# Kernel tuning notes

Hardware: AMD Instinct MI355X
Metric: run time of the kernel (lower is better)

The kernel has to match this reference:

```python
import jax, jax.numpy as jnp
import numpy as np

RES = 64
C_DIM = 64
N_BLOCKS = 4
EPS = 1e-12


def conv2d(x, w, b, pad):
    out = jax.lax.conv_general_dilated(
        x, w, window_strides=(1, 1), padding=[(pad, pad), (pad, pad)],
        dimension_numbers=('NCHW', 'OIHW', 'NCHW'))
    return out + b[None, :, None, None]


def unfold3(x):
    # F.unfold(kernel=3, padding=1): [B,C,H,W] -> [B, C*9, H*W], torch ordering (c, ki, kj)
    B, C, H, W = x.shape
    xp = jnp.pad(x, ((0, 0), (0, 0), (1, 1), (1, 1)))
    patches = jnp.stack([xp[:, :, ki:ki + H, kj:kj + W]
                         for ki in range(3) for kj in range(3)], axis=2)  # [B,C,9,H,W]
    return patches.reshape(B, C * 9, H * W)


def fold3(t, H, W):
    # F.fold(kernel=3, padding=1): sum overlapping patches back to [B,C,H,W]
    B, C9, L = t.shape
    C = C9 // 9
    t = t.reshape(B, C, 3, 3, H, W)
    out = jnp.zeros((B, C, H + 2, W + 2), t.dtype)
    for ki in range(3):
        for kj in range(3):
            out = out.at[:, :, ki:ki + H, kj:kj + W].add(t[:, :, ki, kj])
    return out[:, :, 1:H + 1, 1:W + 1]


def setup_inputs() -> dict:
    key = jax.random.key(0)
    ks = jax.random.split(key, 16)
    B, L, C = 4, RES * RES, C_DIM
    s = 0.05
    inp = {
        'c0': jax.random.normal(ks[0], (B, L, C), jnp.float32),
        'f0': jax.random.normal(ks[1], (B, L, C), jnp.float32),
        'c1': jax.random.normal(ks[2], (B, L, C), jnp.float32),
        'head_w': jax.random.normal(ks[3], (C, C, 5, 5), jnp.float32) * s,
        'head_b': jax.random.normal(ks[4], (C,), jnp.float32) * s,
        'rb_w1': jax.random.normal(ks[5], (N_BLOCKS, C, C, 3, 3), jnp.float32) * s,
        'rb_b1': jax.random.normal(ks[6], (N_BLOCKS, C), jnp.float32) * s,
        'rb_w2': jax.random.normal(ks[7], (N_BLOCKS, C, C, 3, 3), jnp.float32) * s,
        'rb_b2': jax.random.normal(ks[8], (N_BLOCKS, C), jnp.float32) * s,
        'tail_w': jax.random.normal(ks[9], (C, C, 5, 5), jnp.float32) * s,
        'tail_b': jax.random.normal(ks[10], (C,), jnp.float32) * s,
        'sq_w': jax.random.normal(ks[11], (C, 2 * C, 5, 5), jnp.float32) * s,
        'sq_b': jax.random.normal(ks[12], (C,), jnp.float32) * s,
    }
    return inp


def reference(c0, f0, c1, head_w, head_b, rb_w1, rb_b1, rb_w2, rb_b2,
              tail_w, tail_b, sq_w, sq_b):
    B, L, C = c1.shape
    H = W = RES
    c1 = c1.swapaxes(1, 2).reshape(B, C, H, W)
    c0 = c0.swapaxes(1, 2).reshape(B, C, H, W)
    f0 = f0.swapaxes(1, 2).reshape(B, C, H, W)
    Delta_c = c1 - c0

    # --- search_Trans: patch correlation + best-match texture transfer ---
    c1u = unfold3(c1)                       # [B, C9, L]
    c0u = unfold3(c0).swapaxes(1, 2)        # [B, L, C9]
    c0n = c0u / jnp.maximum(jnp.linalg.norm(c0u, axis=2, keepdims=True), EPS)
    c1n = c1u / jnp.maximum(jnp.linalg.norm(c1u, axis=1, keepdims=True), EPS)
    R = jnp.einsum('blk,bkm->blm', c0n, c1n)  # [B, L, L]
    R_star = jnp.max(R, axis=1)               # [B, L]
    R_arg = jnp.argmax(R, axis=1)              # [B, L]
    f0u = unfold3(f0)                          # [B, C9, L]
    Tu = jnp.take_along_axis(f0u, R_arg[:, None, :], axis=2)
    T = fold3(Tu, H, W) / 9.0                  # [B, C, H, W]
    S = R_star.reshape(B, 1, H, W)

    # --- residual conv stack on Delta_c ---
    x1 = conv2d(Delta_c, head_w, head_b, 2)
    x = x1
    for i in range(rb_w1.shape[0]):  # NOTE: original feeds x1 into every block
        h = jax.nn.relu(conv2d(x1, rb_w1[i], rb_b1[i], 1))
        x = conv2d(h, rb_w2[i], rb_b2[i], 1) + x1
    x = conv2d(x, tail_w, tail_b, 2)
    Delta_c_fea = x + x1

    x = conv2d(jnp.concatenate([Delta_c_fea, T], axis=1), sq_w, sq_b, 2)
    out = Delta_c_fea + x * S
    return out.reshape(B, C, L).swapaxes(1, 2)
```

## Files before the change

### kernel.cpp

```cpp
#include <hip/hip_runtime.h>
#include <hip/hip_bf16.h>


#define BATCH 4

typedef unsigned short u16;
typedef unsigned int   u32;
typedef __attribute__((ext_vector_type(8))) short short8;
typedef __attribute__((ext_vector_type(4))) float f32x4;

__device__ __forceinline__ void bsplit2(float a, float b, u32& ho, u32& lo) {
  __hip_bfloat16 ha = __float2bfloat16(a), hb = __float2bfloat16(b);
  float ra = a - __bfloat162float(ha), rb = b - __bfloat162float(hb);
  __hip_bfloat16 la = __float2bfloat16(ra), lb = __float2bfloat16(rb);
  ho = (u32)*(u16*)&ha | ((u32)*(u16*)&hb << 16);
  lo = (u32)*(u16*)&la | ((u32)*(u16*)&lb << 16);
}

__device__ __forceinline__ void gload_lds16(const void* g, void* l) {
  __builtin_amdgcn_global_load_lds((const __attribute__((address_space(1))) void*)g,
                                   (__attribute__((address_space(3))) void*)l, 16, 0, 0);
}

__global__ __launch_bounds__(256) void norm_kernel(const float* __restrict__ ss0,
    const float* __restrict__ ss1, float* __restrict__ inv0, float* __restrict__ inv1)
{
  int tid = blockIdx.x * 256 + threadIdx.x;
  int b = tid >> 12, l = tid & 4095;
  int y = l >> 6, x = l & 63;
  int base = b << 12;
  float s0 = 0.f, s1 = 0.f;
  for (int dy = -1; dy <= 1; ++dy) {
    int yy = y + dy; if (yy < 0 || yy >= 64) continue;
    for (int dx = -1; dx <= 1; ++dx) {
      int xx = x + dx; if (xx < 0 || xx >= 64) continue;
      int ii = base + (yy << 6) + xx;
      s0 += ss0[ii]; s1 += ss1[ii];
    }
  }
  inv0[tid] = 1.f / fmaxf(sqrtf(s0), 1e-12f);
  inv1[tid] = 1.f / fmaxf(sqrtf(s1), 1e-12f);
}

__global__ __launch_bounds__(256) void split_pad_kernel(const float* __restrict__ c0,
    const float* __restrict__ c1, u16* __restrict__ p0h, u16* __restrict__ p0l,
    u16* __restrict__ p1h, u16* __restrict__ p1l,
    float* __restrict__ ss0, float* __restrict__ ss1)
{
  int b = blockIdx.y, t = threadIdx.x;
  int pix = blockIdx.x * 4 + (t >> 6);
  int c = t & 63;
  int py = pix / 66, px = pix - py * 66;
  size_t d = ((size_t)b * 4356 + pix) * 64 + c;
  bool interior = (py >= 1 && py <= 64 && px >= 1 && px <= 64);
  float v0 = 0.f, v1 = 0.f;
  if (interior) {
    size_t s = (((size_t)b << 12) + ((py - 1) << 6) + (px - 1)) * 64 + c;
    v0 = c0[s]; v1 = c1[s];
  }
  __hip_bfloat16 h = __float2bfloat16(v0);
  float r = v0 - __bfloat162float(h);
  __hip_bfloat16 lo = __float2bfloat16(r);
  p0h[d] = *(u16*)&h; p0l[d] = *(u16*)&lo;
  h = __float2bfloat16(v1);
  r = v1 - __bfloat162float(h);
  lo = __float2bfloat16(r);
  p1h[d] = *(u16*)&h; p1l[d] = *(u16*)&lo;
  float s0 = v0 * v0, s1 = v1 * v1;
#pragma unroll
  for (int off = 32; off; off >>= 1) {
    s0 += __shfl_xor(s0, off);
    s1 += __shfl_xor(s1, off);
  }
  if (c == 0 && interior) {
    int sstid = (b << 12) + ((py - 1) << 6) + (px - 1);
    ss0[sstid] = s0;
    ss1[sstid] = s1;
  }
}

__global__ __launch_bounds__(256) void wprep(const float* __restrict__ src,
    u16* __restrict__ wh, u16* __restrict__ wl, int Cin, int KK, int n)
{
  int i = blockIdx.x * 256 + threadIdx.x;
  if (i >= n) return;
  int per = Cin * KK;
  int cout = i / per;
  int rem = i - cout * per;
  int cin = rem / KK;
  int tap = rem - cin * KK;
  float x = src[i];
  __hip_bfloat16 h = __float2bfloat16(x);
  float r = x - __bfloat162float(h);
  __hip_bfloat16 lo = __float2bfloat16(r);
  int d = (tap * 64 + cout) * Cin + cin;
  wh[d] = *(u16*)&h;
  wl[d] = *(u16*)&lo;
}

__global__ __launch_bounds__(256) void corr_mfma(const u16* __restrict__ p0h,
    const u16* __restrict__ p0l, const u16* __restrict__ p1h, const u16* __restrict__ p1l,
    const float* __restrict__ inv0, float* __restrict__ pval, int* __restrict__ pidx)
{
  __shared__ __align__(16) u16 smem[32768];
  int mt = blockIdx.x, lt = blockIdx.y, b = blockIdx.z;
  int t = threadIdx.x;
  int lane = t & 63, w = t >> 6;
  int wl = w >> 1, wm = w & 1;
  int cc = lane & 15, q = lane >> 4;
  const size_t boff = (size_t)b * 278784;
  const u16* msrc = (w == 0) ? p0h : (w == 1) ? p0l : (w == 2) ? p1h : p1l;
  msrc += boff;
  const float* inv0b = inv0 + (b << 12);
  int isB = w >> 1;

  int srow0 = lane >> 2;
  int cs_g  = (lane & 3) ^ ((lane >> 3) & 3);
  int sw    = (cc >> 1) & 3;

  auto stage = [&](int ssub, int sph, u16* dst) {
    int r = sph >> 1, hh = sph & 1;
    int ki = r / 3, kj = r - ki * 3;
    int pb = isB ? (mt << 7) : ((lt << 9) + (ssub << 7));
#pragma unroll
    for (int it = 0; it < 8; ++it) {
      int p = pb + (it << 4) + srow0;
      int ypad = (p >> 6) + ki, xpad = (p & 63) + kj;
      const u16* g = msrc + (((size_t)(ypad * 66 + xpad)) << 6) + (hh << 5) + (cs_g << 3);
      gload_lds16(g, dst + (it << 9));
    }
  };

  float bval[4] = {-1e30f, -1e30f, -1e30f, -1e30f};
  int   bidx[4] = {0, 0, 0, 0};

  stage(0, 0, smem + (w << 12));

  for (int sub = 0; sub < 4; ++sub) {
    int row0 = (lt << 9) + (sub << 7);
    f32x4 acc[4][4];
#pragma unroll
    for (int i = 0; i < 4; ++i)
#pragma unroll
      for (int j = 0; j < 4; ++j) acc[i][j] = (f32x4){0.f, 0.f, 0.f, 0.f};

    for (int ph = 0; ph < 18; ++ph) {
      int g = sub * 18 + ph;
      int nxt = g + 1;
      if (nxt < 72) {
        int np = ph + 1, ns = sub;
        if (np == 18) { np = 0; ++ns; }
        stage(ns, np, smem + ((nxt & 1) << 14) + (w << 12));
        asm volatile("s_waitcnt vmcnt(8)" ::: "memory");
      } else {
        asm volatile("s_waitcnt vmcnt(0)" ::: "memory");
      }
      __builtin_amdgcn_s_barrier();
      __builtin_amdgcn_sched_barrier(0);
      const u16* bb = smem + ((g & 1) << 14);
      short8 afh[4], afl[4], bfh[4], bfl[4];
#pragma unroll
      for (int i = 0; i < 4; ++i) {
        int ra = (((wl << 6) + (i << 4) + cc) << 5) + ((q ^ sw) << 3);
        afh[i] = *(const short8*)(&bb[ra]);
        afl[i] = *(const short8*)(&bb[4096 + ra]);
      }
#pragma unroll
      for (int j = 0; j < 4; ++j) {
        int rb = (((wm << 6) + (j << 4) + cc) << 5) + ((q ^ sw) << 3);
        bfh[j] = *(const short8*)(&bb[8192 + rb]);
        bfl[j] = *(const short8*)(&bb[12288 + rb]);
      }
#pragma unroll
      for (int i = 0; i < 4; ++i)
#pragma unroll
        for (int j = 0; j < 4; ++j) {
          acc[i][j] = __builtin_amdgcn_mfma_f32_16x16x32_bf16(afh[i], bfl[j], acc[i][j], 0, 0, 0);
          acc[i][j] = __builtin_amdgcn_mfma_f32_16x16x32_bf16(afl[i], bfh[j], acc[i][j], 0, 0, 0);
          acc[i][j] = __builtin_amdgcn_mfma_f32_16x16x32_bf16(afh[i], bfh[j], acc[i][j], 0, 0, 0);
        }
      __builtin_amdgcn_sched_barrier(0);
      __builtin_amdgcn_s_barrier();
    }
#pragma unroll
    for (int i = 0; i < 4; ++i) {
#pragma unroll
      for (int rg = 0; rg < 4; ++rg) {
        int l = row0 + (wl << 6) + (i << 4) + (q << 2) + rg;
        float sc = inv0b[l];
#pragma unroll
        for (int j = 0; j < 4; ++j) {
          float v = acc[i][j][rg] * sc;
          if (v > bval[j]) { bval[j] = v; bidx[j] = l; }
        }
      }
    }
  }

  __syncthreads();
  float* lval = (float*)smem;
  int*   lidx = (int*)((char*)smem + 4096);
  int slot = (wl << 2) + q;
#pragma unroll
  for (int j = 0; j < 4; ++j) {
    int col = (wm << 6) + (j << 4) + cc;
    lval[col * 8 + slot] = bval[j];
    lidx[col * 8 + slot] = bidx[j];
  }
  __syncthreads();
  if (t < 128) {
    float bv = -1e30f; int bi = 0x7FFFFFFF;
    for (int s = 0; s < 8; ++s) {
      float v = lval[t * 8 + s]; int id = lidx[t * 8 + s];
      if (v > bv || (v == bv && id < bi)) { bv = v; bi = id; }
    }
    size_t o = (size_t)(((b << 3) + lt) << 12) + (mt << 7) + t;
    pval[o] = bv; pidx[o] = bi;
  }
}

__global__ __launch_bounds__(256) void reduce_kernel(const float* __restrict__ pval,
    const int* __restrict__ pidx, const float* __restrict__ inv1,
    float* __restrict__ S, int* __restrict__ arg)
{
  int tid = blockIdx.x * 256 + threadIdx.x;
  int b = tid >> 12, m = tid & 4095;
  float bv = -1e30f; int bi = 0x7FFFFFFF;
  for (int lt = 0; lt < 8; ++lt) {
    size_t o = (size_t)(((b << 3) + lt) << 12) + m;
    float v = pval[o]; int id = pidx[o];
    if (v > bv || (v == bv && id < bi)) { bv = v; bi = id; }
  }
  S[tid] = bv * inv1[tid];
  arg[tid] = ((unsigned)bi < 4096u) ? bi : 0;
}

__global__ __launch_bounds__(256) void tgather_kernel(const float* __restrict__ f0,
    const int* __restrict__ arg, float* __restrict__ T)
{
  __shared__ int a3[192];
  int y = blockIdx.x, b = blockIdx.y, t = threadIdx.x;
  if (t < 192) {
    int r = t >> 6, xx = t & 63;
    int yy = y + r - 1;
    a3[t] = (yy >= 0 && yy < 64) ? arg[(b << 12) + (yy << 6) + xx] : 0;
  }
  __syncthreads();
  int c = t & 63, pg = t >> 6;
  for (int it = 0; it < 16; ++it) {
    int px = pg + (it << 2);
    float sum = 0.f;
#pragma unroll
    for (int ki = 0; ki < 3; ++ki) {
      int yn = y + 1 - ki;
      if (yn < 0 || yn >= 64) continue;
#pragma unroll
      for (int kj = 0; kj < 3; ++kj) {
        int xn = px + 1 - kj;
        if (xn < 0 || xn >= 64) continue;
        int p = a3[((2 - ki) << 6) + xn];
        int sy = (p >> 6) + ki - 1, sx = (p & 63) + kj - 1;
        if (sy >= 0 && sy < 64 && sx >= 0 && sx < 64)
          sum += f0[((((size_t)b << 12) + (sy << 6) + sx) << 6) + c];
      }
    }
    T[((((size_t)b << 12) + (y << 6) + px)) * 64 + c] = sum * (1.f / 9.f);
  }
}

template<int KS, int CINCH>
__global__ __launch_bounds__(256) void conv_mfma(const float* __restrict__ in0,
    const float* __restrict__ in1, const u16* __restrict__ whp, const u16* __restrict__ wlp,
    const float* __restrict__ bias, float* __restrict__ outp,
    const float* __restrict__ res, const float* __restrict__ smul, int dorelu, int dm)
{
  constexpr int P = KS / 2;
  constexpr int CIN = CINCH * 32;
  constexpr int NKH = CINCH / 2;
  constexpr int NIT = KS * KS * NKH;
  constexpr int AST = 72;
  __shared__ __align__(16) u16 Ah[2][32 * AST], Al[2][32 * AST];
  __shared__ __align__(16) u16 Bh[2][64 * AST], Bl[2][64 * AST];
  int tile = blockIdx.x, b = blockIdx.y;
  int t = threadIdx.x;
  int lane = t & 63, w = t >> 6;
  int wpx = w >> 1, wm = w & 1;
  int cc = lane & 15, q = lane >> 4;
  int ty = tile >> 1, txb = (tile & 1) << 5;
  const size_t abase = (size_t)b << 12;
  f32x4 acc[2];
  acc[0] = (f32x4){0.f, 0.f, 0.f, 0.f};
  acc[1] = (f32x4){0.f, 0.f, 0.f, 0.f};

  uint4 rg[8];
  int arow = t >> 2, acs = t & 3;
  int tb = t - 128;
  int brow = tb >> 1, bhalf = tb & 1;

  auto issue_loads = [&](int itn) {
    int tapn = (NKH == 1) ? itn : (itn >> 1);
    int kh   = (NKH == 1) ? 0 : (itn & 1);
    int ki = tapn / KS, kj = tapn - ki * KS;
    if (t < 128) {
#pragma unroll
      for (int k = 0; k < 8; ++k) rg[k] = make_uint4(0u, 0u, 0u, 0u);
      int iy = ty + ki - P;
      int ix = txb + arow + kj - P;
      if ((unsigned)iy < 64u && (unsigned)ix < 64u) {
        size_t base = (abase + (iy << 6) + ix) << 6;
        int cg = kh * 64 + acs * 16;
        if (dm) {
#pragma unroll
          for (int k = 0; k < 4; ++k) {
            rg[k]     = *(const uint4*)(in0 + base + cg + 4 * k);
            rg[4 + k] = *(const uint4*)(in1 + base + cg + 4 * k);
          }
        } else {
          const float* sp = (CINCH == 4 && kh == 1) ? (in1 + base + (cg - 64))
                                                    : (in0 + base + cg);
#pragma unroll
          for (int k = 0; k < 4; ++k) rg[k] = *(const uint4*)(sp + 4 * k);
        }
      }
    } else {
      size_t so = (size_t)(tapn * 64 + brow) * CIN + kh * 64 + bhalf * 32;
#pragma unroll
      for (int k = 0; k < 4; ++k) {
        rg[k]     = *(const uint4*)&whp[so + 8 * k];
        rg[4 + k] = *(const uint4*)&wlp[so + 8 * k];
      }
    }
  };

  auto write_lds = [&](int cur) {
    if (t < 128) {
      float v[16];
      if (dm) {
#pragma unroll
        for (int k = 0; k < 4; ++k)
#pragma unroll
          for (int e = 0; e < 4; ++e)
            v[k * 4 + e] = __uint_as_float((&rg[4 + k].x)[e]) - __uint_as_float((&rg[k].x)[e]);
      } else {
#pragma unroll
        for (int k = 0; k < 4; ++k)
#pragma unroll
          for (int e = 0; e < 4; ++e)
            v[k * 4 + e] = __uint_as_float((&rg[k].x)[e]);
      }
      uint4 uh0, ul0, uh1, ul1;
      bsplit2(v[0], v[1], uh0.x, ul0.x);
      bsplit2(v[2], v[3], uh0.y, ul0.y);
      bsplit2(v[4], v[5], uh0.z, ul0.z);
      bsplit2(v[6], v[7], uh0.w, ul0.w);
      bsplit2(v[8], v[9], uh1.x, ul1.x);
      bsplit2(v[10], v[11], uh1.y, ul1.y);
      bsplit2(v[12], v[13], uh1.z, ul1.z);
      bsplit2(v[14], v[15], uh1.w, ul1.w);
      int o = arow * AST + acs * 16;
      *(uint4*)&Ah[cur][o]     = uh0;
      *(uint4*)&Ah[cur][o + 8] = uh1;
      *(uint4*)&Al[cur][o]     = ul0;
      *(uint4*)&Al[cur][o + 8] = ul1;
    } else {
      int o = brow * AST + bhalf * 32;
#pragma unroll
      for (int k = 0; k < 4; ++k) {
        *(uint4*)&Bh[cur][o + 8 * k] = rg[k];
        *(uint4*)&Bl[cur][o + 8 * k] = rg[4 + k];
      }
    }
  };

  issue_loads(0);
  for (int it = 0; it < NIT; ++it) {
    int cur = it & 1;
    write_lds(cur);
    if (it + 1 < NIT) issue_loads(it + 1);
    asm volatile("s_waitcnt lgkmcnt(0)" ::: "memory");
    __builtin_amdgcn_s_barrier();
    __builtin_amdgcn_sched_barrier(0);
    short8 afh[2], afl[2], bfh[2][2], bfl[2][2];
#pragma unroll
    for (int ks = 0; ks < 2; ++ks) {
      int ra = ((wpx << 4) + cc) * AST + ks * 32 + (q << 3);
      afh[ks] = *(const short8*)&Ah[cur][ra];
      afl[ks] = *(const short8*)&Al[cur][ra];
#pragma unroll
      for (int j = 0; j < 2; ++j) {
        int rb = ((wm << 5) + (j << 4) + cc) * AST + ks * 32 + (q << 3);
        bfh[j][ks] = *(const short8*)&Bh[cur][rb];
        bfl[j][ks] = *(const short8*)&Bl[cur][rb];
      }
    }
#pragma unroll
    for (int ks = 0; ks < 2; ++ks) {
      acc[0] = __builtin_amdgcn_mfma_f32_16x16x32_bf16(afh[ks], bfl[0][ks], acc[0], 0, 0, 0);
      acc[1] = __builtin_amdgcn_mfma_f32_16x16x32_bf16(afh[ks], bfl[1][ks], acc[1], 0, 0, 0);
      acc[0] = __builtin_amdgcn_mfma_f32_16x16x32_bf16(afl[ks], bfh[0][ks], acc[0], 0, 0, 0);
      acc[1] = __builtin_amdgcn_mfma_f32_16x16x32_bf16(afl[ks], bfh[1][ks], acc[1], 0, 0, 0);
      acc[0] = __builtin_amdgcn_mfma_f32_16x16x32_bf16(afh[ks], bfh[0][ks], acc[0], 0, 0, 0);
      acc[1] = __builtin_amdgcn_mfma_f32_16x16x32_bf16(afh[ks], bfh[1][ks], acc[1], 0, 0, 0);
    }
  }
#pragma unroll
  for (int rgi = 0; rgi < 4; ++rgi) {
    int p = (ty << 6) + txb + (wpx << 4) + (q << 2) + rgi;
#pragma unroll
    for (int j = 0; j < 2; ++j) {
      int cout = (wm << 5) + (j << 4) + cc;
      float v = acc[j][rgi] + bias[cout];
      if (dorelu) v = fmaxf(v, 0.f);
      size_t oi = ((abase + p) << 6) + cout;
      if (smul) v = res[oi] + v * smul[abase + p];
      else if (res) v += res[oi];
      outp[oi] = v;
    }
  }
}

extern "C" void kernel_launch(void* const* d_in, const int* in_sizes, int n_in,
                              void* d_out, int out_size, void* d_ws, size_t ws_size,
                              hipStream_t stream)
{
  (void)in_sizes; (void)n_in; (void)out_size; (void)ws_size;
  const float* c0     = (const float*)d_in[0];
  const float* f0     = (const float*)d_in[1];
  const float* c1     = (const float*)d_in[2];
  const float* head_w = (const float*)d_in[3];
  const float* head_b = (const float*)d_in[4];
  const float* rb_w1  = (const float*)d_in[5];
  const float* rb_b1  = (const float*)d_in[6];
  const float* rb_w2  = (const float*)d_in[7];
  const float* rb_b2  = (const float*)d_in[8];
  const float* tail_w = (const float*)d_in[9];
  const float* tail_b = (const float*)d_in[10];
  const float* sq_w   = (const float*)d_in[11];
  const float* sq_b   = (const float*)d_in[12];
  float* out = (float*)d_out;
  char* ws = (char*)d_ws;

  const size_t OFF_SS0  = 0;
  const size_t OFF_SS1  = 65536;
  const size_t OFF_INV0 = 131072;
  const size_t OFF_INV1 = 196608;
  const size_t OFF_S    = 262144;
  const size_t OFF_ARG  = 327680;
  const size_t OFF_PVAL = 393216;
  const size_t OFF_PIDX = 917504;
  const size_t OFF_WHH  = 1441792;
  const size_t OFF_WHL  = 1646592;
  const size_t OFF_W1H  = 1851392;
  const size_t OFF_W1L  = 1925120;
  const size_t OFF_W2H  = 1998848;
  const size_t OFF_W2L  = 2072576;
  const size_t OFF_WTH  = 2146304;
  const size_t OFF_WTL  = 2351104;
  const size_t OFF_WSH  = 2555904;
  const size_t OFF_WSL  = 2965504;
  const size_t OFF_P0H  = 3375104;
  const size_t OFF_P0L  = OFF_P0H + 2230272;
  const size_t OFF_P1H  = OFF_P0L + 2230272;
  const size_t OFF_P1L  = OFF_P1H + 2230272;
  const size_t OFF_SA   = 3375104;
  const size_t OFF_SB   = 7569408;
  const size_t OFF_SC   = 11763712;

  float* ss0  = (float*)(ws + OFF_SS0);
  float* ss1  = (float*)(ws + OFF_SS1);
  float* inv0 = (float*)(ws + OFF_INV0);
  float* inv1 = (float*)(ws + OFF_INV1);
  float* Sbuf = (float*)(ws + OFF_S);
  int*   argb = (int*)(ws + OFF_ARG);
  float* pval = (float*)(ws + OFF_PVAL);
  int*   pidx = (int*)(ws + OFF_PIDX);
  u16* whh = (u16*)(ws + OFF_WHH); u16* whl = (u16*)(ws + OFF_WHL);
  u16* w1h = (u16*)(ws + OFF_W1H); u16* w1l = (u16*)(ws + OFF_W1L);
  u16* w2h = (u16*)(ws + OFF_W2H); u16* w2l = (u16*)(ws + OFF_W2L);
  u16* wth = (u16*)(ws + OFF_WTH); u16* wtl = (u16*)(ws + OFF_WTL);
  u16* wsh = (u16*)(ws + OFF_WSH); u16* wsl = (u16*)(ws + OFF_WSL);
  u16* p0h = (u16*)(ws + OFF_P0H); u16* p0l = (u16*)(ws + OFF_P0L);
  u16* p1h = (u16*)(ws + OFF_P1H); u16* p1l = (u16*)(ws + OFF_P1L);
  float* x1  = (float*)(ws + OFF_SA);
  float* Tb  = (float*)(ws + OFF_SA);
  float* hb  = (float*)(ws + OFF_SB);
  float* dcf = (float*)(ws + OFF_SB);
  float* xb  = (float*)(ws + OFF_SC);

  dim3 b256(256);
  split_pad_kernel<<<dim3(1089, BATCH), b256, 0, stream>>>(c0, c1, p0h, p0l, p1h, p1l, ss0, ss1);
  norm_kernel<<<dim3(64), b256, 0, stream>>>(ss0, ss1, inv0, inv1);
  wprep<<<dim3(400), b256, 0, stream>>>(head_w, whh, whl, 64, 25, 102400);
  wprep<<<dim3(144), b256, 0, stream>>>(rb_w1 + 110592, w1h, w1l, 64, 9, 36864);
  wprep<<<dim3(144), b256, 0, stream>>>(rb_w2 + 110592, w2h, w2l, 64, 9, 36864);
  wprep<<<dim3(400), b256, 0, stream>>>(tail_w, wth, wtl, 64, 25, 102400);
  wprep<<<dim3(800), b256, 0, stream>>>(sq_w, wsh, wsl, 128, 25, 204800);

  corr_mfma<<<dim3(32, 8, BATCH), b256, 0, stream>>>(p0h, p0l, p1h, p1l, inv0, pval, pidx);
  reduce_kernel<<<dim3(64), b256, 0, stream>>>(pval, pidx, inv1, Sbuf, argb);

  dim3 cgrid(128, BATCH);
  conv_mfma<5, 2><<<cgrid, b256, 0, stream>>>(c0, c1, whh, whl, head_b, x1, nullptr, nullptr, 0, 1);
  conv_mfma<3, 2><<<cgrid, b256, 0, stream>>>(x1, nullptr, w1h, w1l, rb_b1 + 192, hb, nullptr, nullptr, 1, 0);
  conv_mfma<3, 2><<<cgrid, b256, 0, stream>>>(hb, nullptr, w2h, w2l, rb_b2 + 192, xb, x1, nullptr, 0, 0);
  conv_mfma<5, 2><<<cgrid, b256, 0, stream>>>(xb, nullptr, wth, wtl, tail_b, dcf, x1, nullptr, 0, 0);

  tgather_kernel<<<dim3(64, BATCH), b256, 0, stream>>>(f0, argb, Tb);
  conv_mfma<5, 4><<<cgrid, b256, 0, stream>>>(dcf, Tb, wsh, wsl, sq_b, out, dcf, Sbuf, 0, 0);
}
```

Before: 514.4 us.

## Double corr_mfma workgroup to 512 threads, halving per-wave tile and staging

The correlation MFMA kernel now runs 8 waves per workgroup instead of 4. Each wave computes a 32x64 sub-tile instead of 64x64, which halves its accumulator registers, and each pair of waves shares the global-to-LDS staging of one matrix. Staging addresses are precomputed per wave as base pointers plus a per-phase offset, and the MFMA block is wrapped in s_setprio to favour the math waves. The final cross-wave argmax reduction now covers 16 slots per column. The aim is more latency hiding and less register pressure, at the cost of more barrier participants.

```diff
diff --git a/kernel.cpp b/kernel.cpp
--- a/kernel.cpp
+++ b/kernel.cpp
@@ -98,7 +98,7 @@
   wl[d] = *(u16*)&lo;
 }
 
-__global__ __launch_bounds__(256) void corr_mfma(const u16* __restrict__ p0h,
+__global__ __launch_bounds__(512) void corr_mfma(const u16* __restrict__ p0h,
     const u16* __restrict__ p0l, const u16* __restrict__ p1h, const u16* __restrict__ p1l,
     const float* __restrict__ inv0, float* __restrict__ pval, int* __restrict__ pidx)
 {
@@ -106,41 +106,46 @@
   int mt = blockIdx.x, lt = blockIdx.y, b = blockIdx.z;
   int t = threadIdx.x;
   int lane = t & 63, w = t >> 6;
-  int wl = w >> 1, wm = w & 1;
+  int wa = w >> 1, wm = w & 1;
+  int mat = w >> 1, half = w & 1;
   int cc = lane & 15, q = lane >> 4;
   const size_t boff = (size_t)b * 278784;
-  const u16* msrc = (w == 0) ? p0h : (w == 1) ? p0l : (w == 2) ? p1h : p1l;
+  const u16* msrc = (mat == 0) ? p0h : (mat == 1) ? p0l : (mat == 2) ? p1h : p1l;
   msrc += boff;
   const float* inv0b = inv0 + (b << 12);
-  int isB = w >> 1;
+  int isB = mat >> 1;
 
   int srow0 = lane >> 2;
   int cs_g  = (lane & 3) ^ ((lane >> 3) & 3);
   int sw    = (cc >> 1) & 3;
 
-  auto stage = [&](int ssub, int sph, u16* dst) {
+  const u16* gb[4];
+#pragma unroll
+  for (int ii = 0; ii < 4; ++ii) {
+    int k = ((half * 4 + ii) << 4) + srow0;
+    gb[ii] = msrc + ((((k >> 6) * 66) + (k & 63)) << 6) + (cs_g << 3);
+  }
+
+  auto stage = [&](int ssub, int sph, u16* dstbase) {
     int r = sph >> 1, hh = sph & 1;
     int ki = r / 3, kj = r - ki * 3;
-    int pb = isB ? (mt << 7) : ((lt << 9) + (ssub << 7));
-#pragma unroll
-    for (int it = 0; it < 8; ++it) {
-      int p = pb + (it << 4) + srow0;
-      int ypad = (p >> 6) + ki, xpad = (p & 63) + kj;
-      const u16* g = msrc + (((size_t)(ypad * 66 + xpad)) << 6) + (hh << 5) + (cs_g << 3);
-      gload_lds16(g, dst + (it << 9));
-    }
+    int pbr = isB ? (mt << 1) : ((lt << 3) + (ssub << 1));
+    int uoff = (((pbr + ki) * 66 + kj) << 6) + (hh << 5);
+#pragma unroll
+    for (int ii = 0; ii < 4; ++ii)
+      gload_lds16(gb[ii] + uoff, dstbase + ((half * 4 + ii) << 9));
   };
 
   float bval[4] = {-1e30f, -1e30f, -1e30f, -1e30f};
   int   bidx[4] = {0, 0, 0, 0};
 
-  stage(0, 0, smem + (w << 12));
+  stage(0, 0, smem + (mat << 12));
 
   for (int sub = 0; sub < 4; ++sub) {
     int row0 = (lt << 9) + (sub << 7);
-    f32x4 acc[4][4];
-#pragma unroll
-    for (int i = 0; i < 4; ++i)
+    f32x4 acc[2][4];
+#pragma unroll
+    for (int i = 0; i < 2; ++i)
 #pragma unroll
       for (int j = 0; j < 4; ++j) acc[i][j] = (f32x4){0.f, 0.f, 0.f, 0.f};
 
@@ -150,18 +155,18 @@
       if (nxt < 72) {
         int np = ph + 1, ns = sub;
         if (np == 18) { np = 0; ++ns; }
-        stage(ns, np, smem + ((nxt & 1) << 14) + (w << 12));
-        asm volatile("s_waitcnt vmcnt(8)" ::: "memory");
+        stage(ns, np, smem + ((nxt & 1) << 14) + (mat << 12));
+        asm volatile("s_waitcnt vmcnt(4)" ::: "memory");
       } else {
         asm volatile("s_waitcnt vmcnt(0)" ::: "memory");
       }
       __builtin_amdgcn_s_barrier();
       __builtin_amdgcn_sched_barrier(0);
       const u16* bb = smem + ((g & 1) << 14);
-      short8 afh[4], afl[4], bfh[4], bfl[4];
-#pragma unroll
-      for (int i = 0; i < 4; ++i) {
-        int ra = (((wl << 6) + (i << 4) + cc) << 5) + ((q ^ sw) << 3);
+      short8 afh[2], afl[2], bfh[4], bfl[4];
+#pragma unroll
+      for (int i = 0; i < 2; ++i) {
+        int ra = (((wa << 5) + (i << 4) + cc) << 5) + ((q ^ sw) << 3);
         afh[i] = *(const short8*)(&bb[ra]);
         afl[i] = *(const short8*)(&bb[4096 + ra]);
       }
@@ -171,22 +176,24 @@
         bfh[j] = *(const short8*)(&bb[8192 + rb]);
         bfl[j] = *(const short8*)(&bb[12288 + rb]);
       }
-#pragma unroll
-      for (int i = 0; i < 4; ++i)
+      __builtin_amdgcn_s_setprio(1);
+#pragma unroll
+      for (int i = 0; i < 2; ++i)
 #pragma unroll
         for (int j = 0; j < 4; ++j) {
           acc[i][j] = __builtin_amdgcn_mfma_f32_16x16x32_bf16(afh[i], bfl[j], acc[i][j], 0, 0, 0);
           acc[i][j] = __builtin_amdgcn_mfma_f32_16x16x32_bf16(afl[i], bfh[j], acc[i][j], 0, 0, 0);
           acc[i][j] = __builtin_amdgcn_mfma_f32_16x16x32_bf16(afh[i], bfh[j], acc[i][j], 0, 0, 0);
         }
+      __builtin_amdgcn_s_setprio(0);
       __builtin_amdgcn_sched_barrier(0);
       __builtin_amdgcn_s_barrier();
     }
 #pragma unroll
-    for (int i = 0; i < 4; ++i) {
+    for (int i = 0; i < 2; ++i) {
 #pragma unroll
       for (int rg = 0; rg < 4; ++rg) {
-        int l = row0 + (wl << 6) + (i << 4) + (q << 2) + rg;
+        int l = row0 + (wa << 5) + (i << 4) + (q << 2) + rg;
         float sc = inv0b[l];
 #pragma unroll
         for (int j = 0; j < 4; ++j) {
@@ -199,19 +206,19 @@
 
   __syncthreads();
   float* lval = (float*)smem;
-  int*   lidx = (int*)((char*)smem + 4096);
-  int slot = (wl << 2) + q;
+  int*   lidx = (int*)((char*)smem + 8192);
+  int slot = (wa << 2) + q;
 #pragma unroll
   for (int j = 0; j < 4; ++j) {
     int col = (wm << 6) + (j << 4) + cc;
-    lval[col * 8 + slot] = bval[j];
-    lidx[col * 8 + slot] = bidx[j];
+    lval[col * 16 + slot] = bval[j];
+    lidx[col * 16 + slot] = bidx[j];
   }
   __syncthreads();
   if (t < 128) {
     float bv = -1e30f; int bi = 0x7FFFFFFF;
-    for (int s = 0; s < 8; ++s) {
-      float v = lval[t * 8 + s]; int id = lidx[t * 8 + s];
+    for (int s = 0; s < 16; ++s) {
+      float v = lval[t * 16 + s]; int id = lidx[t * 16 + s];
       if (v > bv || (v == bv && id < bi)) { bv = v; bi = id; }
     }
     size_t o = (size_t)(((b << 3) + lt) << 12) + (mt << 7) + t;
@@ -496,7 +503,7 @@
   wprep<<<dim3(400), b256, 0, stream>>>(tail_w, wth, wtl, 64, 25, 102400);
   wprep<<<dim3(800), b256, 0, stream>>>(sq_w, wsh, wsl, 128, 25, 204800);
 
-  corr_mfma<<<dim3(32, 8, BATCH), b256, 0, stream>>>(p0h, p0l, p1h, p1l, inv0, pval, pidx);
+  corr_mfma<<<dim3(32, 8, BATCH), dim3(512), 0, stream>>>(p0h, p0l, p1h, p1l, inv0, pval, pidx);
   reduce_kernel<<<dim3(64), b256, 0, stream>>>(pval, pidx, inv1, Sbuf, argb);
 
   dim3 cgrid(128, BATCH);
```

New measurement: 506.6 us. No clear change (-1.5%).

## Fuse norm and reduce kernels into corr and gather, merge weight prep launches

Applied to the files above, without the earlier changes.

Removes the standalone norm and reduce kernels: corr_mfma now computes the inverse norms for its row tile into LDS from the sums of squares, and tgather reduces the per-tile partial max/argmax and computes S itself. The five weight-prep launches become one kernel that dispatches on block index. Staging address arithmetic is hoisted into precomputed base pointers, and the MFMA loop is wrapped in s_setprio. This cuts launch count and intermediate global traffic, but the inverse norms are now recomputed redundantly in every corr block and the reduce work is repeated three times per pixel in the gather.

```diff
diff --git a/kernel.cpp b/kernel.cpp
--- a/kernel.cpp
+++ b/kernel.cpp
@@ -20,26 +20,6 @@
 __device__ __forceinline__ void gload_lds16(const void* g, void* l) {
   __builtin_amdgcn_global_load_lds((const __attribute__((address_space(1))) void*)g,
                                    (__attribute__((address_space(3))) void*)l, 16, 0, 0);
-}
-
-__global__ __launch_bounds__(256) void norm_kernel(const float* __restrict__ ss0,
-    const float* __restrict__ ss1, float* __restrict__ inv0, float* __restrict__ inv1)
-{
-  int tid = blockIdx.x * 256 + threadIdx.x;
-  int b = tid >> 12, l = tid & 4095;
-  int y = l >> 6, x = l & 63;
-  int base = b << 12;
-  float s0 = 0.f, s1 = 0.f;
-  for (int dy = -1; dy <= 1; ++dy) {
-    int yy = y + dy; if (yy < 0 || yy >= 64) continue;
-    for (int dx = -1; dx <= 1; ++dx) {
-      int xx = x + dx; if (xx < 0 || xx >= 64) continue;
-      int ii = base + (yy << 6) + xx;
-      s0 += ss0[ii]; s1 += ss1[ii];
-    }
-  }
-  inv0[tid] = 1.f / fmaxf(sqrtf(s0), 1e-12f);
-  inv1[tid] = 1.f / fmaxf(sqrtf(s1), 1e-12f);
 }
 
 __global__ __launch_bounds__(256) void split_pad_kernel(const float* __restrict__ c0,
@@ -79,10 +59,21 @@
   }
 }
 
-__global__ __launch_bounds__(256) void wprep(const float* __restrict__ src,
-    u16* __restrict__ wh, u16* __restrict__ wl, int Cin, int KK, int n)
+__global__ __launch_bounds__(256) void wprep_all(
+    const float* __restrict__ hw, u16* __restrict__ whh, u16* __restrict__ whl,
+    const float* __restrict__ r1, u16* __restrict__ w1h, u16* __restrict__ w1l,
+    const float* __restrict__ r2, u16* __restrict__ w2h, u16* __restrict__ w2l,
+    const float* __restrict__ tw, u16* __restrict__ wth, u16* __restrict__ wtl,
+    const float* __restrict__ sw, u16* __restrict__ wsh, u16* __restrict__ wsl)
 {
-  int i = blockIdx.x * 256 + threadIdx.x;
+  int bid = blockIdx.x;
+  const float* src; u16 *wh, *wl; int Cin, KK, n, i;
+  if (bid < 400)       { src = hw; wh = whh; wl = whl; Cin = 64;  KK = 25; n = 102400; i = bid * 256; }
+  else if (bid < 544)  { src = r1; wh = w1h; wl = w1l; Cin = 64;  KK = 9;  n = 36864;  i = (bid - 400) * 256; }
+  else if (bid < 688)  { src = r2; wh = w2h; wl = w2l; Cin = 64;  KK = 9;  n = 36864;  i = (bid - 544) * 256; }
+  else if (bid < 1088) { src = tw; wh = wth; wl = wtl; Cin = 64;  KK = 25; n = 102400; i = (bid - 688) * 256; }
+  else                 { src = sw; wh = wsh; wl = wsl; Cin = 128; KK = 25; n = 204800; i = (bid - 1088) * 256; }
+  i += threadIdx.x;
   if (i >= n) return;
   int per = Cin * KK;
   int cout = i / per;
@@ -100,9 +91,10 @@
 
 __global__ __launch_bounds__(256) void corr_mfma(const u16* __restrict__ p0h,
     const u16* __restrict__ p0l, const u16* __restrict__ p1h, const u16* __restrict__ p1l,
-    const float* __restrict__ inv0, float* __restrict__ pval, int* __restrict__ pidx)
+    const float* __restrict__ ss0, float* __restrict__ pval, int* __restrict__ pidx)
 {
   __shared__ __align__(16) u16 smem[32768];
+  __shared__ float linv[512];
   int mt = blockIdx.x, lt = blockIdx.y, b = blockIdx.z;
   int t = threadIdx.x;
   int lane = t & 63, w = t >> 6;
@@ -111,24 +103,44 @@
   const size_t boff = (size_t)b * 278784;
   const u16* msrc = (w == 0) ? p0h : (w == 1) ? p0l : (w == 2) ? p1h : p1l;
   msrc += boff;
-  const float* inv0b = inv0 + (b << 12);
   int isB = w >> 1;
 
   int srow0 = lane >> 2;
   int cs_g  = (lane & 3) ^ ((lane >> 3) & 3);
   int sw    = (cc >> 1) & 3;
 
+  {
+    const float* ssb = ss0 + (b << 12);
+    for (int r = t; r < 512; r += 256) {
+      int l = (lt << 9) + r;
+      int y = l >> 6, x = l & 63;
+      float s = 0.f;
+      for (int dy = -1; dy <= 1; ++dy) {
+        int yy = y + dy; if ((unsigned)yy >= 64u) continue;
+        for (int dx = -1; dx <= 1; ++dx) {
+          int xx = x + dx; if ((unsigned)xx >= 64u) continue;
+          s += ssb[(yy << 6) + xx];
+        }
+      }
+      linv[r] = 1.f / fmaxf(sqrtf(s), 1e-12f);
+    }
+  }
+
+  const u16* gb[8];
+#pragma unroll
+  for (int ii = 0; ii < 8; ++ii) {
+    int k = (ii << 4) + srow0;
+    gb[ii] = msrc + ((((k >> 6) * 66) + (k & 63)) << 6) + (cs_g << 3);
+  }
+
   auto stage = [&](int ssub, int sph, u16* dst) {
     int r = sph >> 1, hh = sph & 1;
     int ki = r / 3, kj = r - ki * 3;
-    int pb = isB ? (mt << 7) : ((lt << 9) + (ssub << 7));
-#pragma unroll
-    for (int it = 0; it < 8; ++it) {
-      int p = pb + (it << 4) + srow0;
-      int ypad = (p >> 6) + ki, xpad = (p & 63) + kj;
-      const u16* g = msrc + (((size_t)(ypad * 66 + xpad)) << 6) + (hh << 5) + (cs_g << 3);
-      gload_lds16(g, dst + (it << 9));
-    }
+    int pbr = isB ? (mt << 1) : ((lt << 3) + (ssub << 1));
+    int uoff = (((pbr + ki) * 66 + kj) << 6) + (hh << 5);
+#pragma unroll
+    for (int ii = 0; ii < 8; ++ii)
+      gload_lds16(gb[ii] + uoff, dst + (ii << 9));
   };
 
   float bval[4] = {-1e30f, -1e30f, -1e30f, -1e30f};
@@ -171,6 +183,7 @@
         bfh[j] = *(const short8*)(&bb[8192 + rb]);
         bfl[j] = *(const short8*)(&bb[12288 + rb]);
       }
+      __builtin_amdgcn_s_setprio(1);
 #pragma unroll
       for (int i = 0; i < 4; ++i)
 #pragma unroll
@@ -179,6 +192,7 @@
           acc[i][j] = __builtin_amdgcn_mfma_f32_16x16x32_bf16(afl[i], bfh[j], acc[i][j], 0, 0, 0);
           acc[i][j] = __builtin_amdgcn_mfma_f32_16x16x32_bf16(afh[i], bfh[j], acc[i][j], 0, 0, 0);
         }
+      __builtin_amdgcn_s_setprio(0);
       __builtin_amdgcn_sched_barrier(0);
       __builtin_amdgcn_s_barrier();
     }
@@ -186,8 +200,9 @@
     for (int i = 0; i < 4; ++i) {
 #pragma unroll
       for (int rg = 0; rg < 4; ++rg) {
-        int l = row0 + (wl << 6) + (i << 4) + (q << 2) + rg;
-        float sc = inv0b[l];
+        int r = (sub << 7) + (wl << 6) + (i << 4) + (q << 2) + rg;
+        float sc = linv[r];
+        int l = (lt << 9) + r;
 #pragma unroll
         for (int j = 0; j < 4; ++j) {
           float v = acc[i][j][rg] * sc;
@@ -219,31 +234,38 @@
   }
 }
 
-__global__ __launch_bounds__(256) void reduce_kernel(const float* __restrict__ pval,
-    const int* __restrict__ pidx, const float* __restrict__ inv1,
-    float* __restrict__ S, int* __restrict__ arg)
-{
-  int tid = blockIdx.x * 256 + threadIdx.x;
-  int b = tid >> 12, m = tid & 4095;
-  float bv = -1e30f; int bi = 0x7FFFFFFF;
-  for (int lt = 0; lt < 8; ++lt) {
-    size_t o = (size_t)(((b << 3) + lt) << 12) + m;
-    float v = pval[o]; int id = pidx[o];
-    if (v > bv || (v == bv && id < bi)) { bv = v; bi = id; }
-  }
-  S[tid] = bv * inv1[tid];
-  arg[tid] = ((unsigned)bi < 4096u) ? bi : 0;
-}
-
 __global__ __launch_bounds__(256) void tgather_kernel(const float* __restrict__ f0,
-    const int* __restrict__ arg, float* __restrict__ T)
+    const float* __restrict__ pval, const int* __restrict__ pidx,
+    const float* __restrict__ ss1, float* __restrict__ S, float* __restrict__ T)
 {
   __shared__ int a3[192];
   int y = blockIdx.x, b = blockIdx.y, t = threadIdx.x;
   if (t < 192) {
     int r = t >> 6, xx = t & 63;
     int yy = y + r - 1;
-    a3[t] = (yy >= 0 && yy < 64) ? arg[(b << 12) + (yy << 6) + xx] : 0;
+    bool ok = (yy >= 0 && yy < 64);
+    float bv = -1e30f; int bi = 0x7FFFFFFF;
+    if (ok) {
+      int m = (yy << 6) + xx;
+      for (int ltv = 0; ltv < 8; ++ltv) {
+        size_t o = (size_t)(((b << 3) + ltv) << 12) + m;
+        float v = pval[o]; int id = pidx[o];
+        if (v > bv || (v == bv && id < bi)) { bv = v; bi = id; }
+      }
+      if (r == 1) {
+        const float* ssb = ss1 + (b << 12);
+        float s = 0.f;
+        for (int dy = -1; dy <= 1; ++dy) {
+          int y2 = yy + dy; if ((unsigned)y2 >= 64u) continue;
+          for (int dx = -1; dx <= 1; ++dx) {
+            int x2 = xx + dx; if ((unsigned)x2 >= 64u) continue;
+            s += ssb[(y2 << 6) + x2];
+          }
+        }
+        S[(b << 12) + m] = bv / fmaxf(sqrtf(s), 1e-12f);
+      }
+    }
+    a3[t] = (ok && (unsigned)bi < 4096u) ? bi : 0;
   }
   __syncthreads();
   int c = t & 63, pg = t >> 6;
@@ -442,10 +464,7 @@
 
   const size_t OFF_SS0  = 0;
   const size_t OFF_SS1  = 65536;
-  const size_t OFF_INV0 = 131072;
-  const size_t OFF_INV1 = 196608;
   const size_t OFF_S    = 262144;
-  const size_t OFF_ARG  = 327680;
   const size_t OFF_PVAL = 393216;
   const size_t OFF_PIDX = 917504;
   const size_t OFF_WHH  = 1441792;
@@ -468,10 +487,7 @@
 
   float* ss0  = (float*)(ws + OFF_SS0);
   float* ss1  = (float*)(ws + OFF_SS1);
-  float* inv0 = (float*)(ws + OFF_INV0);
-  float* inv1 = (float*)(ws + OFF_INV1);
   float* Sbuf = (float*)(ws + OFF_S);
-  int*   argb = (int*)(ws + OFF_ARG);
   float* pval = (float*)(ws + OFF_PVAL);
   int*   pidx = (int*)(ws + OFF_PIDX);
   u16* whh = (u16*)(ws + OFF_WHH); u16* whl = (u16*)(ws + OFF_WHL);
@@ -489,15 +505,11 @@
 
   dim3 b256(256);
   split_pad_kernel<<<dim3(1089, BATCH), b256, 0, stream>>>(c0, c1, p0h, p0l, p1h, p1l, ss0, ss1);
-  norm_kernel<<<dim3(64), b256, 0, stream>>>(ss0, ss1, inv0, inv1);
-  wprep<<<dim3(400), b256, 0, stream>>>(head_w, whh, whl, 64, 25, 102400);
-  wprep<<<dim3(144), b256, 0, stream>>>(rb_w1 + 110592, w1h, w1l, 64, 9, 36864);
-  wprep<<<dim3(144), b256, 0, stream>>>(rb_w2 + 110592, w2h, w2l, 64, 9, 36864);
-  wprep<<<dim3(400), b256, 0, stream>>>(tail_w, wth, wtl, 64, 25, 102400);
-  wprep<<<dim3(800), b256, 0, stream>>>(sq_w, wsh, wsl, 128, 25, 204800);
-
-  corr_mfma<<<dim3(32, 8, BATCH), b256, 0, stream>>>(p0h, p0l, p1h, p1l, inv0, pval, pidx);
-  reduce_kernel<<<dim3(64), b256, 0, stream>>>(pval, pidx, inv1, Sbuf, argb);
+  wprep_all<<<dim3(1888), b256, 0, stream>>>(head_w, whh, whl,
+      rb_w1 + 110592, w1h, w1l, rb_w2 + 110592, w2h, w2l,
+      tail_w, wth, wtl, sq_w, wsh, wsl);
+
+  corr_mfma<<<dim3(32, 8, BATCH), b256, 0, stream>>>(p0h, p0l, p1h, p1l, ss0, pval, pidx);
 
   dim3 cgrid(128, BATCH);
   conv_mfma<5, 2><<<cgrid, b256, 0, stream>>>(c0, c1, whh, whl, head_b, x1, nullptr, nullptr, 0, 1);
@@ -505,6 +517,6 @@
   conv_mfma<3, 2><<<cgrid, b256, 0, stream>>>(hb, nullptr, w2h, w2l, rb_b2 + 192, xb, x1, nullptr, 0, 0);
   conv_mfma<5, 2><<<cgrid, b256, 0, stream>>>(xb, nullptr, wth, wtl, tail_b, dcf, x1, nullptr, 0, 0);
 
-  tgather_kernel<<<dim3(64, BATCH), b256, 0, stream>>>(f0, argb, Tb);
+  tgather_kernel<<<dim3(64, BATCH), b256, 0, stream>>>(f0, pval, pidx, ss1, Sbuf, Tb);
   conv_mfma<5, 4><<<cgrid, b256, 0, stream>>>(dcf, Tb, wsh, wsl, sq_b, out, dcf, Sbuf, 0, 0);
 }
```

Result: no change. 507.2 us (-1.4%).
